# Kernel optimization log

Measured on AMD Instinct MI355X. Metric: run time of the kernel, lower is better.

Reference implementation:

```python
import jax, jax.numpy as jnp
import numpy as np

B, L, D = 8, 2048, 1024
PAD = 512  # trailing padded positions (zeros) to exercise the two padding masks


def setup_inputs() -> dict:
    key = jax.random.key(0)
    ks = jax.random.split(key, 11)
    q = jax.random.normal(ks[0], (B, L, D), dtype=jnp.float32)
    k = jax.random.normal(ks[1], (B, L, D), dtype=jnp.float32)
    v = jax.random.normal(ks[2], (B, L, D), dtype=jnp.float32)
    # zero-pad trailing positions (module infers masks from zero rows)
    q = q.at[:, L - PAD:, :].set(0.0)
    k = k.at[:, L - PAD:, :].set(0.0)
    v = v.at[:, L - PAD:, :].set(0.0)
    s = 1.0 / np.sqrt(D)
    Wq = jax.random.normal(ks[3], (D, D), dtype=jnp.float32) * s
    bq = jax.random.normal(ks[4], (D,), dtype=jnp.float32) * 0.01
    Wk = jax.random.normal(ks[5], (D, D), dtype=jnp.float32) * s
    bk = jax.random.normal(ks[6], (D,), dtype=jnp.float32) * 0.01
    Wv = jax.random.normal(ks[7], (D, D), dtype=jnp.float32) * s
    bv = jax.random.normal(ks[8], (D,), dtype=jnp.float32) * 0.01
    Wo = jax.random.normal(ks[9], (D, D), dtype=jnp.float32) * s
    bo = jax.random.normal(ks[10], (D,), dtype=jnp.float32) * 0.01
    return {"q": q, "k": k, "v": v, "Wq": Wq, "bq": bq, "Wk": Wk, "bk": bk,
            "Wv": Wv, "bv": bv, "Wo": Wo, "bo": bo}


def reference(q, k, v, Wq, bq, Wk, bk, Wv, bv, Wo, bo):
    # masks computed from raw (pre-projection) q, k, exactly like padding_mask_k/_q
    # bmm(ones_like(q), k^T)[b,i,j] == sum_d k[b,j,d]  -> mask where k row sums to 0
    attn_mask = (jnp.sum(k, axis=-1) == 0.0)[:, None, :]      # [B,1,Lk] -> broadcast [B,Lq,Lk]
    softmax_mask = (jnp.sum(q, axis=-1) == 0.0)[:, :, None]    # [B,Lq,1]

    qp = q @ Wq.T + bq  # torch Linear: x W^T + b
    kp = k @ Wk.T + bk
    vp = v @ Wv.T + bv

    scale = vp.shape[-1] ** -0.5  # original overwrites passed `scale`
    att = jnp.einsum('bqd,bkd->bqk', qp, kp) * scale           # [B,Lq,Lk]
    att = jnp.where(attn_mask, -jnp.inf, att)
    att = jax.nn.softmax(att, axis=-1)
    att = jnp.where(softmax_mask, 0.0, att)

    out = jnp.einsum('bqk,bkd->bqd', att, vp)                  # [B,Lq,D]
    out = out @ Wo.T + bo
    x = out + qp  # residual uses the PROJECTED q
    # LayerNorm, elementwise_affine=False, eps=1e-5
    mu = jnp.mean(x, axis=-1, keepdims=True)
    var = jnp.mean(jnp.square(x - mu), axis=-1, keepdims=True)
    return (x - mu) / jnp.sqrt(var + 1e-5)
```

## Files before the change

kernel.cpp:

```cpp
#include <hip/hip_runtime.h>
#include <stdint.h>

typedef unsigned short u16;
typedef __attribute__((ext_vector_type(8))) short short8;
typedef __attribute__((ext_vector_type(4))) float f32x4;

#define B_ 8
#define L_ 2048
#define D_ 1024

__device__ __forceinline__ u16 f2bf(float f) {
    unsigned int u = __float_as_uint(f);
    u = u + 0x7FFFu + ((u >> 16) & 1u);
    return (u16)(u >> 16);
}
__device__ __forceinline__ float bf2f(u16 h) {
    return __uint_as_float(((unsigned int)h) << 16);
}

struct CM3 {
    const float* s[3];
    u16* d[3];
    int* m[3];
};
__global__ __launch_bounds__(256) void convmask3_kernel(CM3 c) {
    int sel = blockIdx.y;
    const float* x = c.s[sel];
    u16* xb = c.d[sel];
    int* mask = c.m[sel];
    long row = blockIdx.x;
    int t = threadIdx.x;
    float4 v = ((const float4*)(x + row * D_))[t];
    ushort4 o;
    o.x = f2bf(v.x); o.y = f2bf(v.y); o.z = f2bf(v.z); o.w = f2bf(v.w);
    ((ushort4*)(xb + row * D_))[t] = o;
    float s = v.x + v.y + v.z + v.w;
    #pragma unroll
    for (int off = 32; off; off >>= 1) s += __shfl_down(s, off);
    __shared__ float sh[4];
    if ((t & 63) == 0) sh[t >> 6] = s;
    __syncthreads();
    if (t == 0) {
        float tot = sh[0] + sh[1] + sh[2] + sh[3];
        mask[row] = (tot == 0.0f) ? 1 : 0;
    }
}

struct Ptr4 { const float* s0; const float* s1; const float* s2; const float* s3; };
__global__ __launch_bounds__(256) void convert4_kernel(Ptr4 p, u16* __restrict__ dst) {
    const float* srcs[4] = {p.s0, p.s1, p.s2, p.s3};
    const float* src = srcs[blockIdx.y];
    u16* d = dst + (size_t)blockIdx.y * D_ * D_;
    int i = blockIdx.x * 256 + threadIdx.x;
    float4 v = ((const float4*)src)[i];
    ushort4 o;
    o.x = f2bf(v.x); o.y = f2bf(v.y); o.z = f2bf(v.z); o.w = f2bf(v.w);
    ((ushort4*)d)[i] = o;
}

__global__ __launch_bounds__(256) void flags_kernel(const int* __restrict__ mq,
                                                    const int* __restrict__ mk,
                                                    const int* __restrict__ mv,
                                                    int* __restrict__ q256,
                                                    int* __restrict__ k256,
                                                    int* __restrict__ v256,
                                                    int* __restrict__ k128,
                                                    int* __restrict__ k32) {
    int b = blockIdx.x, t = threadIdx.x;
    const int* src; int* dst; int g; int n;
    if (b < 64)       { src = mq; dst = q256; g = b;       n = 256; }
    else if (b < 128) { src = mk; dst = k256; g = b - 64;  n = 256; }
    else if (b < 192) { src = mv; dst = v256; g = b - 128; n = 256; }
    else if (b < 320) { src = mk; dst = k128; g = b - 192; n = 128; }
    else              { src = mk; dst = k32;  g = b - 320; n = 32;  }
    int val = (t < n) ? src[(long)g * n + t] : 1;
    __shared__ int sh;
    if (t == 0) sh = 1;
    __syncthreads();
    if (!val) sh = 0;
    __syncthreads();
    if (t == 0) dst[g] = sh;
}

__global__ __launch_bounds__(512) void packbits_kernel(const int* __restrict__ k32,
                                                       unsigned long long* __restrict__ kb) {
    int t = threadIdx.x;
    int b = t >> 6;
    int bit = t & 63;
    unsigned long long m = __ballot(k32[b * 64 + bit] == 0);
    if (bit == 0) kb[b] = m;
}

__device__ __forceinline__ void async_cp16(const void* g, void* l) {
    __builtin_amdgcn_global_load_lds((const __attribute__((address_space(1))) unsigned int*)g,
                                     (__attribute__((address_space(3))) unsigned int*)l,
                                     16, 0, 0);
}

struct P3 {
    const u16* A[3];
    u16* C[3];
    const float* bias[3];
    const int* rs[3];
};

#define GBM 256
#define GBN 128
#define GBK 32

#define KSTEP(pA, pB)                                                                      \
    do {                                                                                   \
        async_cp16((pA), lA);                                                              \
        async_cp16((pA) + 64 * (long)K, lA + 2048);                                        \
        async_cp16((pA) + 128 * (long)K, lA + 4096);                                       \
        async_cp16((pA) + 192 * (long)K, lA + 6144);                                       \
        async_cp16((pB), lB);                                                              \
        async_cp16((pB) + 64 * (long)K, lB + 2048);                                        \
        __syncthreads();                                                                   \
        short8 af[4], bfr[8];                                                              \
        _Pragma("unroll")                                                                  \
        for (int i = 0; i < 4; i++)                                                        \
            af[i] = *(const short8*)&As[(mrow + i * 16) * GBK + sw];                       \
        _Pragma("unroll")                                                                  \
        for (int j = 0; j < 8; j++)                                                        \
            bfr[j] = *(const short8*)&Bs[((lane & 15) + j * 16) * GBK + sw];               \
        _Pragma("unroll")                                                                  \
        for (int i = 0; i < 4; i++)                                                        \
            _Pragma("unroll")                                                              \
            for (int j = 0; j < 8; j++)                                                    \
                acc[i][j] = __builtin_amdgcn_mfma_f32_16x16x32_bf16(af[i], bfr[j],         \
                                                                    acc[i][j], 0, 0, 0);   \
        __syncthreads();                                                                   \
    } while (0)

template <int MODE>
__global__ __launch_bounds__(256, 2) void gemm_nt(const u16* __restrict__ A,
                                                  const u16* __restrict__ Bm,
                                                  void* __restrict__ C,
                                                  const float* __restrict__ bias,
                                                  const u16* __restrict__ resid,
                                                  const int* __restrict__ maskk,
                                                  int N, int K,
                                                  long strideA, long strideB, long strideC,
                                                  float scale,
                                                  const int* __restrict__ rowskip,
                                                  const int* __restrict__ colskip,
                                                  const unsigned long long* __restrict__ kbits,
                                                  int mblocks, int nblocks,
                                                  P3 p3) {
    __shared__ __align__(16) u16 As[GBM * GBK];
    __shared__ __align__(16) u16 Bs[GBN * GBK];

    int t = threadIdx.x;
    int lane = t & 63;
    int wave = t >> 6;
    long m0 = (long)blockIdx.x * GBM;
    long n0 = (long)blockIdx.y * GBN;

    const u16* Ab;
    const u16* Bb;
    char* Cb;
    const float* biasp = bias;
    const int* rs;
    int rsidx;
    if (MODE == 0) {
        int z = blockIdx.z;
        Ab = p3.A[z];
        Bb = Bm + (long)z * D_ * D_;
        Cb = (char*)p3.C[z];
        biasp = p3.bias[z];
        rs = p3.rs[z];
        rsidx = blockIdx.x;
    } else {
        Ab = A + (long)blockIdx.z * strideA;
        Bb = Bm + (long)blockIdx.z * strideB;
        Cb = (char*)C + (long)blockIdx.z * strideC;
        rs = rowskip;
        rsidx = blockIdx.z * mblocks + blockIdx.x;
    }
    const int* mk = (MODE == 1) ? (maskk + (long)blockIdx.z * N) : nullptr;

    bool skipK = false;
    if (rs && rs[rsidx]) skipK = true;
    if (MODE == 1 && colskip && colskip[blockIdx.z * nblocks + blockIdx.y]) skipK = true;

    f32x4 acc[4][8] = {};

    int arow = t >> 2;
    int acol = ((t & 3) ^ ((t >> 3) & 3)) * 8;
    const u16* gA = Ab + (m0 + arow) * (long)K + acol;
    const u16* gB = Bb + (n0 + arow) * (long)K + acol;
    u16* lA = As + t * 8;
    u16* lB = Bs + t * 8;

    int mrow = wave * 64 + (lane & 15);
    int sw = (((lane >> 4) ^ ((lane >> 1) & 3)) * 8);

    if (!skipK) {
        if (MODE == 2) {
            unsigned long long bits = kbits[blockIdx.z];
            while (bits) {
                int step = __builtin_ctzll(bits);
                bits &= bits - 1;
                const u16* pA = gA + (long)step * GBK;
                const u16* pB = gB + (long)step * GBK;
                KSTEP(pA, pB);
            }
        } else {
            for (int k0 = 0; k0 < K; k0 += GBK) {
                KSTEP(gA, gB);
                gA += GBK;
                gB += GBK;
            }
        }
    }

    long crow0 = m0 + wave * 64;
    long ccol0 = n0;
    #pragma unroll
    for (int i = 0; i < 4; i++) {
        #pragma unroll
        for (int j = 0; j < 8; j++) {
            long row = crow0 + i * 16 + (lane >> 4) * 4;
            long col = ccol0 + j * 16 + (lane & 15);
            #pragma unroll
            for (int r = 0; r < 4; r++) {
                float vv = acc[i][j][r];
                long rr = row + r;
                if (MODE == 0) {
                    ((u16*)Cb)[rr * N + col] = f2bf(vv + biasp[col]);
                } else if (MODE == 1) {
                    float s = mk[col] ? -1e30f : vv * scale;
                    ((u16*)Cb)[rr * N + col] = f2bf(s);
                } else if (MODE == 2) {
                    ((u16*)Cb)[rr * N + col] = f2bf(vv);
                } else {
                    float x = vv + biasp[col] + bf2f(resid[rr * (long)N + col]);
                    ((u16*)Cb)[rr * N + col] = f2bf(x);
                }
            }
        }
    }
}

__global__ __launch_bounds__(256) void softmax_kernel(const u16* __restrict__ S,
                                                      u16* __restrict__ P,
                                                      const int* __restrict__ maskq) {
    long row = blockIdx.x;
    int t = threadIdx.x;
    const u16* Sr = S + row * L_;
    u16* Pr = P + row * L_;

    if (maskq[row]) {
        short8 z = {};
        *(short8*)&Pr[t * 8] = z;
        return;
    }

    short8 raw = *(const short8*)&Sr[t * 8];
    float s[8];
    #pragma unroll
    for (int e = 0; e < 8; e++) s[e] = bf2f((u16)raw[e]);

    float mx = s[0];
    #pragma unroll
    for (int e = 1; e < 8; e++) mx = fmaxf(mx, s[e]);
    #pragma unroll
    for (int off = 32; off; off >>= 1) mx = fmaxf(mx, __shfl_down(mx, off));
    __shared__ float sh[4];
    if ((t & 63) == 0) sh[t >> 6] = mx;
    __syncthreads();
    mx = fmaxf(fmaxf(sh[0], sh[1]), fmaxf(sh[2], sh[3]));
    __syncthreads();

    float e8[8], sum = 0.f;
    #pragma unroll
    for (int e = 0; e < 8; e++) { e8[e] = __expf(s[e] - mx); sum += e8[e]; }
    #pragma unroll
    for (int off = 32; off; off >>= 1) sum += __shfl_down(sum, off);
    if ((t & 63) == 0) sh[t >> 6] = sum;
    __syncthreads();
    sum = sh[0] + sh[1] + sh[2] + sh[3];
    float inv = 1.0f / sum;

    short8 o;
    #pragma unroll
    for (int e = 0; e < 8; e++) o[e] = (short)f2bf(e8[e] * inv);
    *(short8*)&Pr[t * 8] = o;
}

__global__ __launch_bounds__(256) void transpose_k(const u16* __restrict__ src,
                                                   u16* __restrict__ dst) {
    __shared__ u16 tile[32][34];
    long b = blockIdx.z;
    const u16* s = src + b * (long)L_ * D_;
    u16* d = dst + b * (long)L_ * D_;
    int gx = blockIdx.x * 32;
    int gy = blockIdx.y * 32;
    int tx = threadIdx.x, ty = threadIdx.y;
    #pragma unroll
    for (int r = 0; r < 32; r += 8)
        tile[ty + r][tx] = s[(long)(gy + ty + r) * D_ + gx + tx];
    __syncthreads();
    #pragma unroll
    for (int r = 0; r < 32; r += 8)
        d[(long)(gx + ty + r) * L_ + gy + tx] = tile[tx][ty + r];
}

__global__ __launch_bounds__(256) void layernorm_kernel(const u16* __restrict__ X,
                                                        float* __restrict__ O) {
    long row = blockIdx.x;
    int t = threadIdx.x;
    ushort4 u = ((const ushort4*)(X + row * D_))[t];
    float x0 = bf2f(u.x), x1 = bf2f(u.y), x2 = bf2f(u.z), x3 = bf2f(u.w);
    float s = x0 + x1 + x2 + x3;
    #pragma unroll
    for (int off = 32; off; off >>= 1) s += __shfl_down(s, off);
    __shared__ float sh[4];
    if ((t & 63) == 0) sh[t >> 6] = s;
    __syncthreads();
    float mu = (sh[0] + sh[1] + sh[2] + sh[3]) * (1.0f / D_);
    __syncthreads();

    float d0 = x0 - mu, d1 = x1 - mu, d2 = x2 - mu, d3 = x3 - mu;
    float ss = d0 * d0 + d1 * d1 + d2 * d2 + d3 * d3;
    #pragma unroll
    for (int off = 32; off; off >>= 1) ss += __shfl_down(ss, off);
    if ((t & 63) == 0) sh[t >> 6] = ss;
    __syncthreads();
    float var = (sh[0] + sh[1] + sh[2] + sh[3]) * (1.0f / D_);
    float rs = rsqrtf(var + 1e-5f);

    float4 o;
    o.x = d0 * rs; o.y = d1 * rs; o.z = d2 * rs; o.w = d3 * rs;
    ((float4*)(O + row * D_))[t] = o;
}

extern "C" void kernel_launch(void* const* d_in, const int* in_sizes, int n_in,
                              void* d_out, int out_size, void* d_ws, size_t ws_size,
                              hipStream_t stream) {
    const float* q  = (const float*)d_in[0];
    const float* k  = (const float*)d_in[1];
    const float* v  = (const float*)d_in[2];
    const float* Wq = (const float*)d_in[3];
    const float* bq = (const float*)d_in[4];
    const float* Wk = (const float*)d_in[5];
    const float* bk = (const float*)d_in[6];
    const float* Wv = (const float*)d_in[7];
    const float* bv = (const float*)d_in[8];
    const float* Wo = (const float*)d_in[9];
    const float* bo = (const float*)d_in[10];
    float* out = (float*)d_out;

    char* ws = (char*)d_ws;
    const size_t SZ = (size_t)B_ * L_ * D_ * 2;

    u16* qb   = (u16*)(ws + 0 * SZ);
    u16* kb   = (u16*)(ws + 1 * SZ);
    u16* vb   = (u16*)(ws + 2 * SZ);
    u16* vpb  = (u16*)(ws + 3 * SZ);
    u16* Sbuf = (u16*)(ws + 0 * SZ);
    u16* Pbuf = (u16*)(ws + 2 * SZ);
    u16* Obuf = (u16*)(ws + 0 * SZ);
    u16* Xbuf = (u16*)(ws + 2 * SZ);
    char* p = ws + 4 * SZ;
    u16* qpb = (u16*)p; p += SZ;
    u16* kpb = (u16*)p; p += SZ;
    u16* vpT = (u16*)p; p += SZ;
    u16* Wqb = (u16*)p; p += (size_t)D_ * D_ * 2;
    u16* Wkb = (u16*)p; p += (size_t)D_ * D_ * 2;
    u16* Wvb = (u16*)p; p += (size_t)D_ * D_ * 2;
    u16* Wob = (u16*)p; p += (size_t)D_ * D_ * 2;
    int* maskq = (int*)p; p += (size_t)B_ * L_ * 4;
    int* maskk = (int*)p; p += (size_t)B_ * L_ * 4;
    int* maskv = (int*)p; p += (size_t)B_ * L_ * 4;
    int* q256 = (int*)p; p += 64 * 4;
    int* k256 = (int*)p; p += 64 * 4;
    int* v256 = (int*)p; p += 64 * 4;
    int* kmask128 = (int*)p; p += 128 * 4;
    int* kmask32  = (int*)p; p += 512 * 4;
    unsigned long long* kbits = (unsigned long long*)p; p += 8 * 8;

    P3 noP3 = {};

    CM3 cm;
    cm.s[0] = q;  cm.s[1] = k;  cm.s[2] = v;
    cm.d[0] = qb; cm.d[1] = kb; cm.d[2] = vb;
    cm.m[0] = maskq; cm.m[1] = maskk; cm.m[2] = maskv;
    convmask3_kernel<<<dim3(B_ * L_, 3), 256, 0, stream>>>(cm);
    Ptr4 wp{Wq, Wk, Wv, Wo};
    convert4_kernel<<<dim3(D_ * D_ / 4 / 256, 4), 256, 0, stream>>>(wp, Wqb);
    flags_kernel<<<832, 256, 0, stream>>>(maskq, maskk, maskv, q256, k256, v256, kmask128, kmask32);
    packbits_kernel<<<1, 512, 0, stream>>>(kmask32, kbits);

    P3 pj;
    pj.A[0] = qb;  pj.A[1] = kb;  pj.A[2] = vb;
    pj.C[0] = qpb; pj.C[1] = kpb; pj.C[2] = vpb;
    pj.bias[0] = bq; pj.bias[1] = bk; pj.bias[2] = bv;
    pj.rs[0] = q256; pj.rs[1] = k256; pj.rs[2] = v256;
    gemm_nt<0><<<dim3(B_ * L_ / GBM, D_ / GBN, 3), 256, 0, stream>>>(
        nullptr, Wqb, nullptr, nullptr, nullptr, nullptr, D_, D_, 0, 0, 0, 0.f,
        nullptr, nullptr, nullptr, 0, 8, pj);

    transpose_k<<<dim3(D_ / 32, L_ / 32, B_), dim3(32, 8), 0, stream>>>(vpb, vpT);

    gemm_nt<1><<<dim3(L_ / GBM, L_ / GBN, B_), 256, 0, stream>>>(
        qpb, kpb, Sbuf, nullptr, nullptr, maskk, L_, D_,
        (long)L_ * D_, (long)L_ * D_, (long)L_ * L_ * 2, 0.03125f,
        q256, kmask128, nullptr, L_ / GBM, L_ / GBN, noP3);

    softmax_kernel<<<B_ * L_, 256, 0, stream>>>(Sbuf, Pbuf, maskq);

    gemm_nt<2><<<dim3(L_ / GBM, D_ / GBN, B_), 256, 0, stream>>>(
        Pbuf, vpT, Obuf, nullptr, nullptr, nullptr, D_, L_,
        (long)L_ * L_, (long)D_ * L_, (long)L_ * D_ * 2, 0.f,
        q256, nullptr, kbits, L_ / GBM, D_ / GBN, noP3);

    gemm_nt<3><<<dim3(B_ * L_ / GBM, D_ / GBN, 1), 256, 0, stream>>>(
        Obuf, Wob, Xbuf, bo, qpb, nullptr, D_, D_, 0, 0, 0, 0.f,
        q256, nullptr, nullptr, B_ * L_ / GBM, D_ / GBN, noP3);

    layernorm_kernel<<<B_ * L_, 256, 0, stream>>>(Xbuf, out);
}
```

Before: 583.9 us.

## Pipeline GEMM with 4-slot async LDS ring and 256x256 tiles on 512 threads

Rewrites the shared bf16 GEMM kernel so global-to-LDS async copies run three k-steps ahead in a four-slot ring buffer. Fine-grained vmcnt waits and a single barrier per step replace the old two-barrier load-then-compute loop. The output tile grows to 256x256 with 8 waves per block, each owning a 128x64 sub-tile, and s_setprio is raised around the MFMA bursts. The column-skip table for the score GEMM is switched to the 256-granularity k mask to match the wider tile. This trades 128 KB of LDS per block and more registers for load latency hiding and higher data reuse, which may cut occupancy.

```diff
diff --git a/kernel.cpp b/kernel.cpp
--- a/kernel.cpp
+++ b/kernel.cpp
@@ -105,36 +105,22 @@
 };
 
 #define GBM 256
-#define GBN 128
+#define GBN 256
 #define GBK 32
 
-#define KSTEP(pA, pB)                                                                      \
-    do {                                                                                   \
-        async_cp16((pA), lA);                                                              \
-        async_cp16((pA) + 64 * (long)K, lA + 2048);                                        \
-        async_cp16((pA) + 128 * (long)K, lA + 4096);                                       \
-        async_cp16((pA) + 192 * (long)K, lA + 6144);                                       \
-        async_cp16((pB), lB);                                                              \
-        async_cp16((pB) + 64 * (long)K, lB + 2048);                                        \
-        __syncthreads();                                                                   \
-        short8 af[4], bfr[8];                                                              \
-        _Pragma("unroll")                                                                  \
-        for (int i = 0; i < 4; i++)                                                        \
-            af[i] = *(const short8*)&As[(mrow + i * 16) * GBK + sw];                       \
-        _Pragma("unroll")                                                                  \
-        for (int j = 0; j < 8; j++)                                                        \
-            bfr[j] = *(const short8*)&Bs[((lane & 15) + j * 16) * GBK + sw];               \
-        _Pragma("unroll")                                                                  \
-        for (int i = 0; i < 4; i++)                                                        \
-            _Pragma("unroll")                                                              \
-            for (int j = 0; j < 8; j++)                                                    \
-                acc[i][j] = __builtin_amdgcn_mfma_f32_16x16x32_bf16(af[i], bfr[j],         \
-                                                                    acc[i][j], 0, 0, 0);   \
-        __syncthreads();                                                                   \
+#define STAGE(step, slot)                                                   \
+    do {                                                                    \
+        const u16* pa_ = gA + (long)(step) * GBK;                           \
+        const u16* pb_ = gB + (long)(step) * GBK;                           \
+        u16* la_ = &LDS[(slot)][0] + t * 8;                                 \
+        async_cp16(pa_, la_);                                               \
+        async_cp16(pa_ + 128 * (long)K, la_ + 4096);                        \
+        async_cp16(pb_, la_ + 8192);                                        \
+        async_cp16(pb_ + 128 * (long)K, la_ + 12288);                       \
     } while (0)
 
 template <int MODE>
-__global__ __launch_bounds__(256, 2) void gemm_nt(const u16* __restrict__ A,
+__global__ __launch_bounds__(512, 2) void gemm_nt(const u16* __restrict__ A,
                                                   const u16* __restrict__ Bm,
                                                   void* __restrict__ C,
                                                   const float* __restrict__ bias,
@@ -148,12 +134,13 @@
                                                   const unsigned long long* __restrict__ kbits,
                                                   int mblocks, int nblocks,
                                                   P3 p3) {
-    __shared__ __align__(16) u16 As[GBM * GBK];
-    __shared__ __align__(16) u16 Bs[GBN * GBK];
+    __shared__ __align__(16) u16 LDS[4][16384];
 
     int t = threadIdx.x;
     int lane = t & 63;
     int wave = t >> 6;
+    int wr = wave >> 2;
+    int wc = wave & 3;
     long m0 = (long)blockIdx.x * GBM;
     long n0 = (long)blockIdx.y * GBN;
 
@@ -184,43 +171,87 @@
     if (rs && rs[rsidx]) skipK = true;
     if (MODE == 1 && colskip && colskip[blockIdx.z * nblocks + blockIdx.y]) skipK = true;
 
-    f32x4 acc[4][8] = {};
-
-    int arow = t >> 2;
-    int acol = ((t & 3) ^ ((t >> 3) & 3)) * 8;
-    const u16* gA = Ab + (m0 + arow) * (long)K + acol;
-    const u16* gB = Bb + (n0 + arow) * (long)K + acol;
-    u16* lA = As + t * 8;
-    u16* lB = Bs + t * 8;
-
-    int mrow = wave * 64 + (lane & 15);
-    int sw = (((lane >> 4) ^ ((lane >> 1) & 3)) * 8);
+    f32x4 acc[8][4] = {};
+
+    int srow = t >> 2;
+    int kc = ((t & 3) ^ ((t >> 3) & 3)) * 8;
+    const u16* gA = Ab + (m0 + srow) * (long)K + kc;
+    const u16* gB = Bb + (n0 + srow) * (long)K + kc;
+
+    int sw = ((lane >> 4) ^ ((lane >> 1) & 3)) * 8;
+    int arow0 = wr * 128 + (lane & 15);
+    int brow0 = wc * 64 + (lane & 15);
 
     if (!skipK) {
+        unsigned long long bs = 0;
+        int NT;
         if (MODE == 2) {
-            unsigned long long bits = kbits[blockIdx.z];
-            while (bits) {
-                int step = __builtin_ctzll(bits);
-                bits &= bits - 1;
-                const u16* pA = gA + (long)step * GBK;
-                const u16* pB = gB + (long)step * GBK;
-                KSTEP(pA, pB);
+            bs = kbits[blockIdx.z];
+            NT = __popcll(bs);
+        } else {
+            NT = K / GBK;
+        }
+
+        int npro = NT < 3 ? NT : 3;
+        for (int i = 0; i < npro; i++) {
+            int st = i;
+            if (MODE == 2) { st = __builtin_ctzll(bs); bs &= bs - 1; }
+            STAGE(st, i);
+        }
+        int nstaged = npro;
+
+        for (int tt = 0; tt < NT; tt++) {
+            int rem = NT - 1 - tt;
+            if (rem > 1)      asm volatile("s_waitcnt vmcnt(8)" ::: "memory");
+            else if (rem == 1) asm volatile("s_waitcnt vmcnt(4)" ::: "memory");
+            else               asm volatile("s_waitcnt vmcnt(0)" ::: "memory");
+            __builtin_amdgcn_s_barrier();
+            asm volatile("" ::: "memory");
+
+            if (nstaged < NT) {
+                int st = nstaged;
+                if (MODE == 2) { st = __builtin_ctzll(bs); bs &= bs - 1; }
+                STAGE(st, nstaged & 3);
+                nstaged++;
             }
-        } else {
-            for (int k0 = 0; k0 < K; k0 += GBK) {
-                KSTEP(gA, gB);
-                gA += GBK;
-                gB += GBK;
-            }
+
+            const u16* As_ = &LDS[tt & 3][0];
+            const u16* Bs_ = As_ + 8192;
+            short8 bfr[4], af[4];
+            #pragma unroll
+            for (int j = 0; j < 4; j++)
+                bfr[j] = *(const short8*)&Bs_[(brow0 + j * 16) * GBK + sw];
+            #pragma unroll
+            for (int i = 0; i < 4; i++)
+                af[i] = *(const short8*)&As_[(arow0 + i * 16) * GBK + sw];
+            __builtin_amdgcn_s_setprio(1);
+            #pragma unroll
+            for (int i = 0; i < 4; i++)
+                #pragma unroll
+                for (int j = 0; j < 4; j++)
+                    acc[i][j] = __builtin_amdgcn_mfma_f32_16x16x32_bf16(af[i], bfr[j],
+                                                                        acc[i][j], 0, 0, 0);
+            __builtin_amdgcn_s_setprio(0);
+            #pragma unroll
+            for (int i = 0; i < 4; i++)
+                af[i] = *(const short8*)&As_[(arow0 + 64 + i * 16) * GBK + sw];
+            __builtin_amdgcn_s_setprio(1);
+            #pragma unroll
+            for (int i = 0; i < 4; i++)
+                #pragma unroll
+                for (int j = 0; j < 4; j++)
+                    acc[4 + i][j] = __builtin_amdgcn_mfma_f32_16x16x32_bf16(af[i], bfr[j],
+                                                                            acc[4 + i][j], 0, 0, 0);
+            __builtin_amdgcn_s_setprio(0);
         }
     }
 
-    long crow0 = m0 + wave * 64;
-    long ccol0 = n0;
-    #pragma unroll
-    for (int i = 0; i < 4; i++) {
+    long crow0 = m0 + wr * 128;
+    long ccol0 = n0 + wc * 64;
+    #pragma unroll
+    for (int i = 0; i < 8; i++) {
         #pragma unroll
-        for (int j = 0; j < 8; j++) {
+        for (int j = 0; j < 4; j++) {
             long row = crow0 + i * 16 + (lane >> 4) * 4;
             long col = ccol0 + j * 16 + (lane & 15);
             #pragma unroll
@@ -398,25 +429,25 @@
     pj.C[0] = qpb; pj.C[1] = kpb; pj.C[2] = vpb;
     pj.bias[0] = bq; pj.bias[1] = bk; pj.bias[2] = bv;
     pj.rs[0] = q256; pj.rs[1] = k256; pj.rs[2] = v256;
-    gemm_nt<0><<<dim3(B_ * L_ / GBM, D_ / GBN, 3), 256, 0, stream>>>(
+    gemm_nt<0><<<dim3(B_ * L_ / GBM, D_ / GBN, 3), 512, 0, stream>>>(
         nullptr, Wqb, nullptr, nullptr, nullptr, nullptr, D_, D_, 0, 0, 0, 0.f,
-        nullptr, nullptr, nullptr, 0, 8, pj);
+        nullptr, nullptr, nullptr, 0, 4, pj);
 
     transpose_k<<<dim3(D_ / 32, L_ / 32, B_), dim3(32, 8), 0, stream>>>(vpb, vpT);
 
-    gemm_nt<1><<<dim3(L_ / GBM, L_ / GBN, B_), 256, 0, stream>>>(
+    gemm_nt<1><<<dim3(L_ / GBM, L_ / GBN, B_), 512, 0, stream>>>(
         qpb, kpb, Sbuf, nullptr, nullptr, maskk, L_, D_,
         (long)L_ * D_, (long)L_ * D_, (long)L_ * L_ * 2, 0.03125f,
-        q256, kmask128, nullptr, L_ / GBM, L_ / GBN, noP3);
+        q256, k256, nullptr, L_ / GBM, L_ / GBN, noP3);
 
     softmax_kernel<<<B_ * L_, 256, 0, stream>>>(Sbuf, Pbuf, maskq);
 
-    gemm_nt<2><<<dim3(L_ / GBM, D_ / GBN, B_), 256, 0, stream>>>(
+    gemm_nt<2><<<dim3(L_ / GBM, D_ / GBN, B_), 512, 0, stream>>>(
         Pbuf, vpT, Obuf, nullptr, nullptr, nullptr, D_, L_,
         (long)L_ * L_, (long)D_ * L_, (long)L_ * D_ * 2, 0.f,
         q256, nullptr, kbits, L_ / GBM, D_ / GBN, noP3);
 
-    gemm_nt<3><<<dim3(B_ * L_ / GBM, D_ / GBN, 1), 256, 0, stream>>>(
+    gemm_nt<3><<<dim3(B_ * L_ / GBM, D_ / GBN, 1), 512, 0, stream>>>(
         Obuf, Wob, Xbuf, bo, qpb, nullptr, D_, D_, 0, 0, 0, 0.f,
         q256, nullptr, nullptr, B_ * L_ / GBM, D_ / GBN, noP3);
 
```

Measured after the change: 550.7 us. 1.06x faster.

## Double-buffer GEMM LDS tiles and shrink block tile to 128x128 with 2x2 waves

Applied to the files above, without the earlier changes.

Reworks the shared bf16 GEMM kernel to use 128x128 block tiles with a 2x2 wave layout in place of 256x128 with four row-stacked waves. The LDS tiles are double-buffered so the async global-to-LDS copy of the next K step is issued before computing the current one, which drops one barrier per step. Occupancy is raised to 3 blocks per CU, and the row-skip flags are recomputed at 128-row granularity to match the new tile. The aim is to hide load latency and get more blocks in flight, at the cost of lower per-wave MFMA reuse (4x4 instead of 4x8 accumulators) and more total blocks.

```diff
diff --git a/kernel.cpp b/kernel.cpp
--- a/kernel.cpp
+++ b/kernel.cpp
@@ -61,18 +61,16 @@
 __global__ __launch_bounds__(256) void flags_kernel(const int* __restrict__ mq,
                                                     const int* __restrict__ mk,
                                                     const int* __restrict__ mv,
-                                                    int* __restrict__ q256,
-                                                    int* __restrict__ k256,
-                                                    int* __restrict__ v256,
+                                                    int* __restrict__ q128,
                                                     int* __restrict__ k128,
+                                                    int* __restrict__ v128,
                                                     int* __restrict__ k32) {
     int b = blockIdx.x, t = threadIdx.x;
     const int* src; int* dst; int g; int n;
-    if (b < 64)       { src = mq; dst = q256; g = b;       n = 256; }
-    else if (b < 128) { src = mk; dst = k256; g = b - 64;  n = 256; }
-    else if (b < 192) { src = mv; dst = v256; g = b - 128; n = 256; }
-    else if (b < 320) { src = mk; dst = k128; g = b - 192; n = 128; }
-    else              { src = mk; dst = k32;  g = b - 320; n = 32;  }
+    if (b < 128)      { src = mq; dst = q128; g = b;       n = 128; }
+    else if (b < 256) { src = mk; dst = k128; g = b - 128; n = 128; }
+    else if (b < 384) { src = mv; dst = v128; g = b - 256; n = 128; }
+    else              { src = mk; dst = k32;  g = b - 384; n = 32;  }
     int val = (t < n) ? src[(long)g * n + t] : 1;
     __shared__ int sh;
     if (t == 0) sh = 1;
@@ -104,37 +102,22 @@
     const int* rs[3];
 };
 
-#define GBM 256
+#define GBM 128
 #define GBN 128
 #define GBK 32
 
-#define KSTEP(pA, pB)                                                                      \
-    do {                                                                                   \
-        async_cp16((pA), lA);                                                              \
-        async_cp16((pA) + 64 * (long)K, lA + 2048);                                        \
-        async_cp16((pA) + 128 * (long)K, lA + 4096);                                       \
-        async_cp16((pA) + 192 * (long)K, lA + 6144);                                       \
-        async_cp16((pB), lB);                                                              \
-        async_cp16((pB) + 64 * (long)K, lB + 2048);                                        \
-        __syncthreads();                                                                   \
-        short8 af[4], bfr[8];                                                              \
-        _Pragma("unroll")                                                                  \
-        for (int i = 0; i < 4; i++)                                                        \
-            af[i] = *(const short8*)&As[(mrow + i * 16) * GBK + sw];                       \
-        _Pragma("unroll")                                                                  \
-        for (int j = 0; j < 8; j++)                                                        \
-            bfr[j] = *(const short8*)&Bs[((lane & 15) + j * 16) * GBK + sw];               \
-        _Pragma("unroll")                                                                  \
-        for (int i = 0; i < 4; i++)                                                        \
-            _Pragma("unroll")                                                              \
-            for (int j = 0; j < 8; j++)                                                    \
-                acc[i][j] = __builtin_amdgcn_mfma_f32_16x16x32_bf16(af[i], bfr[j],         \
-                                                                    acc[i][j], 0, 0, 0);   \
-        __syncthreads();                                                                   \
+#define STAGE(BUF, STEP)                                            \
+    do {                                                            \
+        const u16* pa_ = gA + (long)(STEP) * GBK;                   \
+        const u16* pb_ = gB + (long)(STEP) * GBK;                   \
+        async_cp16(pa_, &As[BUF][t * 8]);                           \
+        async_cp16(pa_ + 64 * (long)K, &As[BUF][t * 8 + 2048]);     \
+        async_cp16(pb_, &Bs[BUF][t * 8]);                           \
+        async_cp16(pb_ + 64 * (long)K, &Bs[BUF][t * 8 + 2048]);     \
     } while (0)
 
 template <int MODE>
-__global__ __launch_bounds__(256, 2) void gemm_nt(const u16* __restrict__ A,
+__global__ __launch_bounds__(256, 3) void gemm_nt(const u16* __restrict__ A,
                                                   const u16* __restrict__ Bm,
                                                   void* __restrict__ C,
                                                   const float* __restrict__ bias,
@@ -148,12 +131,14 @@
                                                   const unsigned long long* __restrict__ kbits,
                                                   int mblocks, int nblocks,
                                                   P3 p3) {
-    __shared__ __align__(16) u16 As[GBM * GBK];
-    __shared__ __align__(16) u16 Bs[GBN * GBK];
+    __shared__ __align__(16) u16 As[2][GBM * GBK];
+    __shared__ __align__(16) u16 Bs[2][GBN * GBK];
 
     int t = threadIdx.x;
     int lane = t & 63;
     int wave = t >> 6;
+    int wr = wave >> 1;
+    int wc = wave & 1;
     long m0 = (long)blockIdx.x * GBM;
     long n0 = (long)blockIdx.y * GBN;
 
@@ -184,48 +169,66 @@
     if (rs && rs[rsidx]) skipK = true;
     if (MODE == 1 && colskip && colskip[blockIdx.z * nblocks + blockIdx.y]) skipK = true;
 
-    f32x4 acc[4][8] = {};
+    f32x4 acc[4][4] = {};
 
     int arow = t >> 2;
     int acol = ((t & 3) ^ ((t >> 3) & 3)) * 8;
     const u16* gA = Ab + (m0 + arow) * (long)K + acol;
     const u16* gB = Bb + (n0 + arow) * (long)K + acol;
-    u16* lA = As + t * 8;
-    u16* lB = Bs + t * 8;
-
-    int mrow = wave * 64 + (lane & 15);
-    int sw = (((lane >> 4) ^ ((lane >> 1) & 3)) * 8);
+
+    int mrow = wr * 64 + (lane & 15);
+    int brow = wc * 64 + (lane & 15);
+    int sw = ((lane >> 4) ^ ((lane >> 1) & 3)) * 8;
 
     if (!skipK) {
+        unsigned long long bs = 0;
+        int NT;
         if (MODE == 2) {
-            unsigned long long bits = kbits[blockIdx.z];
-            while (bits) {
-                int step = __builtin_ctzll(bits);
-                bits &= bits - 1;
-                const u16* pA = gA + (long)step * GBK;
-                const u16* pB = gB + (long)step * GBK;
-                KSTEP(pA, pB);
-            }
+            bs = kbits[blockIdx.z];
+            NT = __popcll(bs);
         } else {
-            for (int k0 = 0; k0 < K; k0 += GBK) {
-                KSTEP(gA, gB);
-                gA += GBK;
-                gB += GBK;
+            NT = K / GBK;
+        }
+
+        if (NT > 0) {
+            int st;
+            if (MODE == 2) { st = __builtin_ctzll(bs); bs &= bs - 1; } else st = 0;
+            STAGE(0, st);
+
+            for (int i = 0; i < NT; i++) {
+                __syncthreads();
+                if (i + 1 < NT) {
+                    int stn;
+                    if (MODE == 2) { stn = __builtin_ctzll(bs); bs &= bs - 1; } else stn = i + 1;
+                    STAGE((i + 1) & 1, stn);
+                }
+                int b = i & 1;
+                short8 af[4], bfr[4];
+                #pragma unroll
+                for (int ii = 0; ii < 4; ii++)
+                    af[ii] = *(const short8*)&As[b][(mrow + ii * 16) * GBK + sw];
+                #pragma unroll
+                for (int jj = 0; jj < 4; jj++)
+                    bfr[jj] = *(const short8*)&Bs[b][(brow + jj * 16) * GBK + sw];
+                #pragma unroll
+                for (int ii = 0; ii < 4; ii++)
+                    #pragma unroll
+                    for (int jj = 0; jj < 4; jj++)
+                        acc[ii][jj] = __builtin_amdgcn_mfma_f32_16x16x32_bf16(
+                            af[ii], bfr[jj], acc[ii][jj], 0, 0, 0);
             }
         }
     }
 
-    long crow0 = m0 + wave * 64;
-    long ccol0 = n0;
-    #pragma unroll
-    for (int i = 0; i < 4; i++) {
+    #pragma unroll
+    for (int ii = 0; ii < 4; ii++) {
         #pragma unroll
-        for (int j = 0; j < 8; j++) {
-            long row = crow0 + i * 16 + (lane >> 4) * 4;
-            long col = ccol0 + j * 16 + (lane & 15);
+        for (int jj = 0; jj < 4; jj++) {
+            long row = m0 + wr * 64 + ii * 16 + (lane >> 4) * 4;
+            long col = n0 + wc * 64 + jj * 16 + (lane & 15);
             #pragma unroll
             for (int r = 0; r < 4; r++) {
-                float vv = acc[i][j][r];
+                float vv = acc[ii][jj][r];
                 long rr = row + r;
                 if (MODE == 0) {
                     ((u16*)Cb)[rr * N + col] = f2bf(vv + biasp[col]);
@@ -374,11 +377,10 @@
     int* maskq = (int*)p; p += (size_t)B_ * L_ * 4;
     int* maskk = (int*)p; p += (size_t)B_ * L_ * 4;
     int* maskv = (int*)p; p += (size_t)B_ * L_ * 4;
-    int* q256 = (int*)p; p += 64 * 4;
-    int* k256 = (int*)p; p += 64 * 4;
-    int* v256 = (int*)p; p += 64 * 4;
-    int* kmask128 = (int*)p; p += 128 * 4;
-    int* kmask32  = (int*)p; p += 512 * 4;
+    int* q128 = (int*)p; p += 128 * 4;
+    int* k128 = (int*)p; p += 128 * 4;
+    int* v128 = (int*)p; p += 128 * 4;
+    int* kmask32 = (int*)p; p += 512 * 4;
     unsigned long long* kbits = (unsigned long long*)p; p += 8 * 8;
 
     P3 noP3 = {};
@@ -390,14 +392,14 @@
     convmask3_kernel<<<dim3(B_ * L_, 3), 256, 0, stream>>>(cm);
     Ptr4 wp{Wq, Wk, Wv, Wo};
     convert4_kernel<<<dim3(D_ * D_ / 4 / 256, 4), 256, 0, stream>>>(wp, Wqb);
-    flags_kernel<<<832, 256, 0, stream>>>(maskq, maskk, maskv, q256, k256, v256, kmask128, kmask32);
+    flags_kernel<<<896, 256, 0, stream>>>(maskq, maskk, maskv, q128, k128, v128, kmask32);
     packbits_kernel<<<1, 512, 0, stream>>>(kmask32, kbits);
 
     P3 pj;
     pj.A[0] = qb;  pj.A[1] = kb;  pj.A[2] = vb;
     pj.C[0] = qpb; pj.C[1] = kpb; pj.C[2] = vpb;
     pj.bias[0] = bq; pj.bias[1] = bk; pj.bias[2] = bv;
-    pj.rs[0] = q256; pj.rs[1] = k256; pj.rs[2] = v256;
+    pj.rs[0] = q128; pj.rs[1] = k128; pj.rs[2] = v128;
     gemm_nt<0><<<dim3(B_ * L_ / GBM, D_ / GBN, 3), 256, 0, stream>>>(
         nullptr, Wqb, nullptr, nullptr, nullptr, nullptr, D_, D_, 0, 0, 0, 0.f,
         nullptr, nullptr, nullptr, 0, 8, pj);
@@ -407,18 +409,18 @@
     gemm_nt<1><<<dim3(L_ / GBM, L_ / GBN, B_), 256, 0, stream>>>(
         qpb, kpb, Sbuf, nullptr, nullptr, maskk, L_, D_,
         (long)L_ * D_, (long)L_ * D_, (long)L_ * L_ * 2, 0.03125f,
-        q256, kmask128, nullptr, L_ / GBM, L_ / GBN, noP3);
+        q128, k128, nullptr, L_ / GBM, L_ / GBN, noP3);
 
     softmax_kernel<<<B_ * L_, 256, 0, stream>>>(Sbuf, Pbuf, maskq);
 
     gemm_nt<2><<<dim3(L_ / GBM, D_ / GBN, B_), 256, 0, stream>>>(
         Pbuf, vpT, Obuf, nullptr, nullptr, nullptr, D_, L_,
         (long)L_ * L_, (long)D_ * L_, (long)L_ * D_ * 2, 0.f,
-        q256, nullptr, kbits, L_ / GBM, D_ / GBN, noP3);
+        q128, nullptr, kbits, L_ / GBM, D_ / GBN, noP3);
 
     gemm_nt<3><<<dim3(B_ * L_ / GBM, D_ / GBN, 1), 256, 0, stream>>>(
         Obuf, Wob, Xbuf, bo, qpb, nullptr, D_, D_, 0, 0, 0, 0.f,
-        q256, nullptr, nullptr, B_ * L_ / GBM, D_ / GBN, noP3);
+        q128, nullptr, nullptr, B_ * L_ / GBM, D_ / GBN, noP3);
 
     layernorm_kernel<<<B_ * L_, 256, 0, stream>>>(Xbuf, out);
 }
```

New measurement: 593.9 us. No clear change (+1.7%).
